# Performance work log

Measured on AMD Instinct MI355X. Metric: run time of the kernel, lower is better.

Reference implementation:

```python
import jax, jax.numpy as jnp
import numpy as np

B, S, L = 128, 512, 20  # batch, max seq length, g.max_word_length
VOCAB = 10000


def setup_inputs() -> dict:
    key = jax.random.key(0)
    k1, k2, k3 = jax.random.split(key, 3)
    lost_unit_id_seqs = jax.random.randint(k1, (B, S), 0, VOCAB, dtype=jnp.int32)
    # lengths in [L, S] so every batch element has viable spans
    lost_lengths = jax.random.randint(k2, (B,), L, S + 1, dtype=jnp.int32)
    p_weights = jax.random.uniform(k3, (B, S, L), dtype=jnp.float32)
    return {
        "lost_unit_id_seqs": lost_unit_id_seqs,
        "lost_lengths": lost_lengths,
        "p_weights": p_weights,
        "max_word_length": L,
    }


def reference(lost_unit_id_seqs, lost_lengths, p_weights, max_word_length):
    b, s = lost_unit_id_seqs.shape
    l = max_word_length
    n = b * s * l  # static upper bound on number of viable spans

    # _propose_candidates: enumerate all (start, span_length) pairs
    starts = jnp.arange(s, dtype=jnp.int32)[None, :, None]          # [1,S,1]
    lens = jnp.arange(1, l + 1, dtype=jnp.int32)[None, None, :]      # [1,1,L]
    ends = starts + lens - 1                                          # [1,S,L]

    viable = ends < lost_lengths[:, None, None]                       # [B,S,L] bool
    shape = viable.shape
    start_candidates = jnp.broadcast_to(starts, shape)
    end_candidates = jnp.broadcast_to(ends, shape)
    len_candidates = jnp.broadcast_to(lens, shape)
    batch_indices = jnp.broadcast_to(
        jnp.arange(b, dtype=jnp.int32)[:, None, None], shape)

    # boolean-mask stream compaction with static size (viable entries first,
    # tail padded with index 0; true count = viable.sum())
    flat_viable = viable.reshape(-1)
    idx = jnp.nonzero(flat_viable, size=n, fill_value=0)[0]           # [N]

    viable_starts = start_candidates.reshape(-1)[idx]
    viable_ends = end_candidates.reshape(-1)[idx]
    viable_lengths = len_candidates.reshape(-1)[idx]
    viable_batch_indices = batch_indices.reshape(-1)[idx]
    viable_p_weights = p_weights.reshape(-1)[idx]

    # 2D advanced-index gather of unit ids for each viable span
    max_length = jnp.max(lost_lengths)
    word_pos = jnp.minimum(
        viable_starts[:, None] + jnp.arange(l, dtype=jnp.int32)[None, :],
        max_length - 1)                                               # [N,L]
    viable_unit_id_seqs = lost_unit_id_seqs[viable_batch_indices[:, None], word_pos]

    return (viable, viable_batch_indices, viable_starts, viable_ends,
            viable_lengths, viable_unit_id_seqs, viable_p_weights,
            start_candidates, end_candidates, len_candidates)
```

## Files before the change

### kernel.cpp

```cpp
#include <hip/hip_runtime.h>
#include <stdint.h>

#define TPB 256
#define BB  128
#define SS  512
#define LLW 20
#define NN  (BB * SS * LLW)
#define KPT 4
#define KPB (TPB * KPT)
#define MAXROWS 8
#define RSTRIDE 516

static __device__ __forceinline__ void preamble(const int* __restrict__ lens,
                                                int* shC, int* shM, int* shLen,
                                                int t) {
  int len0 = (t < BB) ? lens[t] : 0;
  shLen[t] = len0;
  shC[t] = (t < BB) ? (LLW * len0 - (LLW * (LLW - 1)) / 2) : 0;
  shM[t] = len0;
  for (int off = 1; off < TPB; off <<= 1) {
    __syncthreads();
    int aC = shC[t]; int bC = (t >= off) ? shC[t - off] : 0;
    int aM = shM[t]; int bM = shM[t ^ off];
    __syncthreads();
    shC[t] = aC + bC;
    shM[t] = (aM > bM) ? aM : bM;
  }
  __syncthreads();
}

static __device__ __forceinline__ int batch_of(int k, const int* shC) {
  int lo = 0, hi = BB - 1;
  while (lo < hi) {
    int mid = (lo + hi) >> 1;
    if (shC[mid] > k) hi = mid; else lo = mid + 1;
  }
  return lo;
}

static __device__ __forceinline__ void invert(int k, const int* shC,
                                              const int* shLen, int K,
                                              int* pb, int* ps, int* pj) {
  int b = 0, s = 0, j = 0;
  if (k < K) {
    b = batch_of(k, shC);
    int base = (b == 0) ? 0 : shC[b - 1];
    int m    = k - base;
    int lenb = shLen[b];
    int full = LLW * (lenb - LLW + 1);
    if (m < full) {
      s = m / LLW;
      j = m - s * LLW;
    } else {
      int Cb = shC[b] - base;
      int tt = Cb - m;
      float rf = (sqrtf(8.0f * (float)tt + 1.0f) - 1.0f) * 0.5f;
      int r = (int)(rf + 0.5f);
      if (r * (r + 1) / 2 < tt) r++;
      if (r > 1 && r * (r - 1) / 2 >= tt) r--;
      s = lenb - r;
      j = r * (r + 1) / 2 - tt;
    }
  }
  *pb = b; *ps = s; *pj = j;
}

__global__ __launch_bounds__(TPB) void span_full(
    const int* __restrict__ seqs,
    const int* __restrict__ lens,
    const float* __restrict__ pw,
    float* __restrict__ out) {
  __shared__ int shC[TPB], shM[TPB], shLen[TPB];
  __shared__ int sBS[KPB];
  __shared__ int sRows[MAXROWS * RSTRIDE];
  const int t = threadIdx.x;
  preamble(lens, shC, shM, shLen, t);
  const int K  = shC[BB - 1];
  const int ml = shM[0];

  const int gid    = blockIdx.x * TPB + t;
  const int k0     = gid * KPT;
  const int blk_k0 = blockIdx.x * KPB;
  const size_t Nz  = (size_t)NN;

  int kq0 = blk_k0;           if (kq0 > K - 1) kq0 = K - 1;
  int kq1 = blk_k0 + KPB - 1; if (kq1 > K - 1) kq1 = K - 1;
  const int bf = batch_of(kq0, shC);
  int nrows = (blk_k0 < K) ? (batch_of(kq1, shC) - bf + 1) : 0;
  if (nrows > MAXROWS) nrows = MAXROWS;
  {
    const int4* src = (const int4*)(seqs + (size_t)bf * SS);
    for (int q = t; q < nrows * (SS / 4); q += TPB) {
      int lin = q << 2;
      int r = lin >> 9, p = lin & (SS - 1);
      *(int4*)(sRows + r * RSTRIDE + p) = src[q];
    }
  }

  {
    float qv[KPT], qsc[KPT], qec[KPT], qlc[KPT];
#pragma unroll
    for (int i = 0; i < KPT; i++) {
      int f   = k0 + i;
      int row = f / LLW;
      int jj  = f - row * LLW;
      int b2  = row >> 9;
      int s2  = row & (SS - 1);
      int e2  = s2 + jj;
      qv[i]  = (e2 < shLen[b2]) ? 1.0f : 0.0f;
      qsc[i] = (float)s2; qec[i] = (float)e2; qlc[i] = (float)(jj + 1);
    }
    *(float4*)(out + k0)           = make_float4(qv[0], qv[1], qv[2], qv[3]);
    *(float4*)(out + 26 * Nz + k0) = make_float4(qsc[0], qsc[1], qsc[2], qsc[3]);
    *(float4*)(out + 27 * Nz + k0) = make_float4(qec[0], qec[1], qec[2], qec[3]);
    *(float4*)(out + 28 * Nz + k0) = make_float4(qlc[0], qlc[1], qlc[2], qlc[3]);
  }
  {
    int b, s, j;
    invert(k0, shC, shLen, K, &b, &s, &j);
    float qb[KPT], qs[KPT], qe[KPT], ql[KPT], qp[KPT];
#pragma unroll
    for (int i = 0; i < KPT; i++) {
      int ki = k0 + i;
      int vb = 0, vs = 0, vj = 0;
      if (ki < K) {
        vb = b; vs = s; vj = j;
        j++;
        int lenb = shLen[b];
        int cs = lenb - s; if (cs > LLW) cs = LLW;
        if (j >= cs) { j = 0; s++; if (s >= lenb) { s = 0; b++; } }
      }
      qb[i] = (float)vb; qs[i] = (float)vs;
      qe[i] = (float)(vs + vj); ql[i] = (float)(vj + 1);
      qp[i] = pw[((size_t)vb * SS + vs) * LLW + vj];
      sBS[t * KPT + i] = (vb << 16) | vs;
    }
    *(float4*)(out + Nz + k0)      = make_float4(qb[0], qb[1], qb[2], qb[3]);
    *(float4*)(out + 2 * Nz + k0)  = make_float4(qs[0], qs[1], qs[2], qs[3]);
    *(float4*)(out + 3 * Nz + k0)  = make_float4(qe[0], qe[1], qe[2], qe[3]);
    *(float4*)(out + 4 * Nz + k0)  = make_float4(ql[0], ql[1], ql[2], ql[3]);
    *(float4*)(out + 25 * Nz + k0) = make_float4(qp[0], qp[1], qp[2], qp[3]);
  }
  __syncthreads();
  {
    int ml1 = ml - 1;
    float4* udst = (float4*)(out + 5 * Nz + (size_t)blk_k0 * LLW);
    for (int c = 0; c < (KPB * (LLW / 4)) / TPB; c++) {
      int chunk = t + c * TPB;
      int krow  = chunk / 5;
      int e0    = (chunk - krow * 5) << 2;
      int bs    = sBS[krow];
      int b = bs >> 16, s = bs & 0xFFFF;
      int p0 = s + e0;     if (p0 > ml1) p0 = ml1;
      int p1 = s + e0 + 1; if (p1 > ml1) p1 = ml1;
      int p2 = s + e0 + 2; if (p2 > ml1) p2 = ml1;
      int p3 = s + e0 + 3; if (p3 > ml1) p3 = ml1;
      float4 v;
      int ridx = b - bf;
      if ((unsigned)ridx < (unsigned)nrows) {
        const int* rp = sRows + ridx * RSTRIDE;
        v.x = (float)rp[p0]; v.y = (float)rp[p1];
        v.z = (float)rp[p2]; v.w = (float)rp[p3];
      } else {
        const int* rp = seqs + (size_t)b * SS;
        v.x = (float)rp[p0]; v.y = (float)rp[p1];
        v.z = (float)rp[p2]; v.w = (float)rp[p3];
      }
      udst[chunk] = v;
    }
  }
}

extern "C" void kernel_launch(void* const* d_in, const int* in_sizes, int n_in,
                              void* d_out, int out_size, void* d_ws, size_t ws_size,
                              hipStream_t stream) {
  const int*   seqs = (const int*)d_in[0];
  const int*   lens = (const int*)d_in[1];
  const float* pw   = (const float*)d_in[2];
  float* out = (float*)d_out;

  span_full<<<NN / KPB, TPB, 0, stream>>>(seqs, lens, pw, out);
}
```

Measured before the change: 161.9 us.

## Split fused span kernel into candidate, scalar, and unit-gather kernels

Splits the single fused kernel into three launches. The first writes the candidate grids, the second computes the compacted scalars and p_weights and stores packed (batch,start) pairs to workspace, and the third gathers the unit IDs from that workspace. The first two kernels now handle 8 elements per thread instead of 4. The aim is to shrink per-block shared memory and register pressure so occupancy rises. In exchange it adds two kernel launches, a workspace round-trip, and a repeat of the prefix-scan preamble in two kernels.

```diff
diff --git a/kernel.cpp b/kernel.cpp
--- a/kernel.cpp
+++ b/kernel.cpp
@@ -6,8 +6,8 @@
 #define SS  512
 #define LLW 20
 #define NN  (BB * SS * LLW)
-#define KPT 4
-#define KPB (TPB * KPT)
+#define FPT 8
+#define KPB3 1024
 #define MAXROWS 8
 #define RSTRIDE 516
 
@@ -65,26 +65,99 @@
   *pb = b; *ps = s; *pj = j;
 }
 
-__global__ __launch_bounds__(TPB) void span_full(
-    const int* __restrict__ seqs,
-    const int* __restrict__ lens,
-    const float* __restrict__ pw,
-    float* __restrict__ out) {
+__global__ __launch_bounds__(TPB) void k_cand(const int* __restrict__ lens,
+                                              float* __restrict__ out) {
+  __shared__ int shLen[BB];
+  const int t = threadIdx.x;
+  if (t < BB) shLen[t] = lens[t];
+  __syncthreads();
+  const size_t Nz = (size_t)NN;
+  const int f0 = (blockIdx.x * TPB + t) * FPT;
+  float qv[FPT], qsc[FPT], qec[FPT], qlc[FPT];
+#pragma unroll
+  for (int i = 0; i < FPT; i++) {
+    int f   = f0 + i;
+    int row = f / LLW;
+    int jj  = f - row * LLW;
+    int b   = row >> 9;
+    int s   = row & (SS - 1);
+    int e   = s + jj;
+    qv[i]  = (e < shLen[b]) ? 1.0f : 0.0f;
+    qsc[i] = (float)s; qec[i] = (float)e; qlc[i] = (float)(jj + 1);
+  }
+#pragma unroll
+  for (int h = 0; h < FPT / 4; h++) {
+    int o = 4 * h;
+    *(float4*)(out + f0 + o)           = make_float4(qv[o], qv[o+1], qv[o+2], qv[o+3]);
+    *(float4*)(out + 26 * Nz + f0 + o) = make_float4(qsc[o], qsc[o+1], qsc[o+2], qsc[o+3]);
+    *(float4*)(out + 27 * Nz + f0 + o) = make_float4(qec[o], qec[o+1], qec[o+2], qec[o+3]);
+    *(float4*)(out + 28 * Nz + f0 + o) = make_float4(qlc[o], qlc[o+1], qlc[o+2], qlc[o+3]);
+  }
+}
+
+__global__ __launch_bounds__(TPB) void k_scal(const int* __restrict__ lens,
+                                              const float* __restrict__ pw,
+                                              float* __restrict__ out,
+                                              int* __restrict__ wsbs) {
   __shared__ int shC[TPB], shM[TPB], shLen[TPB];
-  __shared__ int sBS[KPB];
+  const int t = threadIdx.x;
+  preamble(lens, shC, shM, shLen, t);
+  const int K = shC[BB - 1];
+  const size_t Nz = (size_t)NN;
+  const int k0 = (blockIdx.x * TPB + t) * FPT;
+
+  int b, s, j;
+  invert(k0, shC, shLen, K, &b, &s, &j);
+  float qb[FPT], qs[FPT], qe[FPT], ql[FPT], qp[FPT];
+  int qbs[FPT];
+#pragma unroll
+  for (int i = 0; i < FPT; i++) {
+    int ki = k0 + i;
+    int vb = 0, vs = 0, vj = 0;
+    if (ki < K) {
+      vb = b; vs = s; vj = j;
+      j++;
+      int lenb = shLen[b];
+      int cs = lenb - s; if (cs > LLW) cs = LLW;
+      if (j >= cs) { j = 0; s++; if (s >= lenb) { s = 0; b++; } }
+    }
+    qb[i] = (float)vb; qs[i] = (float)vs;
+    qe[i] = (float)(vs + vj); ql[i] = (float)(vj + 1);
+    qp[i] = pw[((size_t)vb * SS + vs) * LLW + vj];
+    qbs[i] = (vb << 16) | vs;
+  }
+#pragma unroll
+  for (int h = 0; h < FPT / 4; h++) {
+    int o = 4 * h;
+    *(float4*)(out + Nz + k0 + o)      = make_float4(qb[o], qb[o+1], qb[o+2], qb[o+3]);
+    *(float4*)(out + 2 * Nz + k0 + o)  = make_float4(qs[o], qs[o+1], qs[o+2], qs[o+3]);
+    *(float4*)(out + 3 * Nz + k0 + o)  = make_float4(qe[o], qe[o+1], qe[o+2], qe[o+3]);
+    *(float4*)(out + 4 * Nz + k0 + o)  = make_float4(ql[o], ql[o+1], ql[o+2], ql[o+3]);
+    *(float4*)(out + 25 * Nz + k0 + o) = make_float4(qp[o], qp[o+1], qp[o+2], qp[o+3]);
+    *(int4*)(wsbs + k0 + o)            = make_int4(qbs[o], qbs[o+1], qbs[o+2], qbs[o+3]);
+  }
+}
+
+__global__ __launch_bounds__(TPB) void k_units(const int* __restrict__ seqs,
+                                               const int* __restrict__ lens,
+                                               const int* __restrict__ wsbs,
+                                               float* __restrict__ out) {
+  __shared__ int shC[TPB], shM[TPB], shLen[TPB];
+  __shared__ int sBS[KPB3];
   __shared__ int sRows[MAXROWS * RSTRIDE];
   const int t = threadIdx.x;
   preamble(lens, shC, shM, shLen, t);
   const int K  = shC[BB - 1];
   const int ml = shM[0];
-
-  const int gid    = blockIdx.x * TPB + t;
-  const int k0     = gid * KPT;
-  const int blk_k0 = blockIdx.x * KPB;
-  const size_t Nz  = (size_t)NN;
-
-  int kq0 = blk_k0;           if (kq0 > K - 1) kq0 = K - 1;
-  int kq1 = blk_k0 + KPB - 1; if (kq1 > K - 1) kq1 = K - 1;
+  const int blk_k0 = blockIdx.x * KPB3;
+  const size_t Nz = (size_t)NN;
+
+  {
+    const int4* src = (const int4*)(wsbs + blk_k0);
+    ((int4*)sBS)[t] = src[t];
+  }
+  int kq0 = blk_k0;            if (kq0 > K - 1) kq0 = K - 1;
+  int kq1 = blk_k0 + KPB3 - 1; if (kq1 > K - 1) kq1 = K - 1;
   const int bf = batch_of(kq0, shC);
   int nrows = (blk_k0 < K) ? (batch_of(kq1, shC) - bf + 1) : 0;
   if (nrows > MAXROWS) nrows = MAXROWS;
@@ -96,78 +169,32 @@
       *(int4*)(sRows + r * RSTRIDE + p) = src[q];
     }
   }
-
-  {
-    float qv[KPT], qsc[KPT], qec[KPT], qlc[KPT];
-#pragma unroll
-    for (int i = 0; i < KPT; i++) {
-      int f   = k0 + i;
-      int row = f / LLW;
-      int jj  = f - row * LLW;
-      int b2  = row >> 9;
-      int s2  = row & (SS - 1);
-      int e2  = s2 + jj;
-      qv[i]  = (e2 < shLen[b2]) ? 1.0f : 0.0f;
-      qsc[i] = (float)s2; qec[i] = (float)e2; qlc[i] = (float)(jj + 1);
-    }
-    *(float4*)(out + k0)           = make_float4(qv[0], qv[1], qv[2], qv[3]);
-    *(float4*)(out + 26 * Nz + k0) = make_float4(qsc[0], qsc[1], qsc[2], qsc[3]);
-    *(float4*)(out + 27 * Nz + k0) = make_float4(qec[0], qec[1], qec[2], qec[3]);
-    *(float4*)(out + 28 * Nz + k0) = make_float4(qlc[0], qlc[1], qlc[2], qlc[3]);
-  }
-  {
-    int b, s, j;
-    invert(k0, shC, shLen, K, &b, &s, &j);
-    float qb[KPT], qs[KPT], qe[KPT], ql[KPT], qp[KPT];
-#pragma unroll
-    for (int i = 0; i < KPT; i++) {
-      int ki = k0 + i;
-      int vb = 0, vs = 0, vj = 0;
-      if (ki < K) {
-        vb = b; vs = s; vj = j;
-        j++;
-        int lenb = shLen[b];
-        int cs = lenb - s; if (cs > LLW) cs = LLW;
-        if (j >= cs) { j = 0; s++; if (s >= lenb) { s = 0; b++; } }
-      }
-      qb[i] = (float)vb; qs[i] = (float)vs;
-      qe[i] = (float)(vs + vj); ql[i] = (float)(vj + 1);
-      qp[i] = pw[((size_t)vb * SS + vs) * LLW + vj];
-      sBS[t * KPT + i] = (vb << 16) | vs;
-    }
-    *(float4*)(out + Nz + k0)      = make_float4(qb[0], qb[1], qb[2], qb[3]);
-    *(float4*)(out + 2 * Nz + k0)  = make_float4(qs[0], qs[1], qs[2], qs[3]);
-    *(float4*)(out + 3 * Nz + k0)  = make_float4(qe[0], qe[1], qe[2], qe[3]);
-    *(float4*)(out + 4 * Nz + k0)  = make_float4(ql[0], ql[1], ql[2], ql[3]);
-    *(float4*)(out + 25 * Nz + k0) = make_float4(qp[0], qp[1], qp[2], qp[3]);
-  }
   __syncthreads();
-  {
-    int ml1 = ml - 1;
-    float4* udst = (float4*)(out + 5 * Nz + (size_t)blk_k0 * LLW);
-    for (int c = 0; c < (KPB * (LLW / 4)) / TPB; c++) {
-      int chunk = t + c * TPB;
-      int krow  = chunk / 5;
-      int e0    = (chunk - krow * 5) << 2;
-      int bs    = sBS[krow];
-      int b = bs >> 16, s = bs & 0xFFFF;
-      int p0 = s + e0;     if (p0 > ml1) p0 = ml1;
-      int p1 = s + e0 + 1; if (p1 > ml1) p1 = ml1;
-      int p2 = s + e0 + 2; if (p2 > ml1) p2 = ml1;
-      int p3 = s + e0 + 3; if (p3 > ml1) p3 = ml1;
-      float4 v;
-      int ridx = b - bf;
-      if ((unsigned)ridx < (unsigned)nrows) {
-        const int* rp = sRows + ridx * RSTRIDE;
-        v.x = (float)rp[p0]; v.y = (float)rp[p1];
-        v.z = (float)rp[p2]; v.w = (float)rp[p3];
-      } else {
-        const int* rp = seqs + (size_t)b * SS;
-        v.x = (float)rp[p0]; v.y = (float)rp[p1];
-        v.z = (float)rp[p2]; v.w = (float)rp[p3];
-      }
-      udst[chunk] = v;
-    }
+
+  int ml1 = ml - 1;
+  float4* udst = (float4*)(out + 5 * Nz + (size_t)blk_k0 * LLW);
+  for (int c = 0; c < (KPB3 * (LLW / 4)) / TPB; c++) {
+    int chunk = t + c * TPB;
+    int krow  = chunk / 5;
+    int e0    = (chunk - krow * 5) << 2;
+    int bs    = sBS[krow];
+    int b = bs >> 16, s = bs & 0xFFFF;
+    int p0 = s + e0;     if (p0 > ml1) p0 = ml1;
+    int p1 = s + e0 + 1; if (p1 > ml1) p1 = ml1;
+    int p2 = s + e0 + 2; if (p2 > ml1) p2 = ml1;
+    int p3 = s + e0 + 3; if (p3 > ml1) p3 = ml1;
+    float4 v;
+    int ridx = b - bf;
+    if ((unsigned)ridx < (unsigned)nrows) {
+      const int* rp = sRows + ridx * RSTRIDE;
+      v.x = (float)rp[p0]; v.y = (float)rp[p1];
+      v.z = (float)rp[p2]; v.w = (float)rp[p3];
+    } else {
+      const int* rp = seqs + (size_t)b * SS;
+      v.x = (float)rp[p0]; v.y = (float)rp[p1];
+      v.z = (float)rp[p2]; v.w = (float)rp[p3];
+    }
+    udst[chunk] = v;
   }
 }
 
@@ -178,6 +205,9 @@
   const int*   lens = (const int*)d_in[1];
   const float* pw   = (const float*)d_in[2];
   float* out = (float*)d_out;
-
-  span_full<<<NN / KPB, TPB, 0, stream>>>(seqs, lens, pw, out);
-}
+  int*   wsbs = (int*)d_ws;
+
+  k_cand <<<NN / (TPB * FPT), TPB, 0, stream>>>(lens, out);
+  k_scal <<<NN / (TPB * FPT), TPB, 0, stream>>>(lens, pw, out, wsbs);
+  k_units<<<NN / KPB3,        TPB, 0, stream>>>(seqs, lens, wsbs, out);
+}
```

Measured after the change: 173.0 us. 1.07x slower.
